# Kernel tuning notes

Hardware: AMD Instinct MI355X
Metric: run time of the kernel (lower is better)

The kernel has to match this reference:

```python
import jax, jax.numpy as jnp
import numpy as np

B, T, D, H = 2, 2048, 2048, 16
HD = D // H  # 128
HALF = HD // 2  # 64


def _apply_rotary(x, cos, sin):
    """x: (B,H,T,HD); cos/sin: (T, HD//2). Interleaved rotation matching torch ref."""
    half = x.shape[-1] // 2
    x1, x2 = x[..., :half], x[..., half:]
    c = cos[None, None, :, :]
    s = sin[None, None, :, :]
    # stack on last axis then flatten -> out[...,2i]=x1*c-x2*s, out[...,2i+1]=x1*s+x2*c
    return jnp.stack([x1 * c - x2 * s, x1 * s + x2 * c], axis=-1).reshape(x.shape)


def setup_inputs() -> dict:
    key = jax.random.key(0)
    k1, k2, k3 = jax.random.split(key, 3)
    x = jax.random.normal(k1, (B, T, D), dtype=jnp.float32)
    # realistic RoPE tables: theta = 10000^{-2i/HD}
    inv_freq = 1.0 / (10000.0 ** (np.arange(0, HALF, dtype=np.float32) * 2.0 / HD))
    ang = np.arange(T, dtype=np.float32)[:, None] * inv_freq[None, :]  # (T, HALF)
    cos = jnp.asarray(np.cos(ang), dtype=jnp.float32)
    sin = jnp.asarray(np.sin(ang), dtype=jnp.float32)
    Wqkv = jax.random.normal(k2, (D, 3 * D), dtype=jnp.float32) * (D ** -0.5)
    Wproj = jax.random.normal(k3, (D, D), dtype=jnp.float32) * (D ** -0.5)
    return {"x": x, "cos": cos, "sin": sin, "Wqkv": Wqkv, "Wproj": Wproj}


def reference(x, cos, sin, Wqkv, Wproj):
    b, t, d = x.shape
    qkv = (x @ Wqkv).reshape(b, t, 3, H, HD)
    q = jnp.transpose(qkv[:, :, 0], (0, 2, 1, 3))  # (B,H,T,HD)
    k = jnp.transpose(qkv[:, :, 1], (0, 2, 1, 3))
    v = jnp.transpose(qkv[:, :, 2], (0, 2, 1, 3))
    q = _apply_rotary(q, cos, sin)
    k = _apply_rotary(k, cos, sin)
    scale = 1.0 / jnp.sqrt(jnp.asarray(HD, dtype=x.dtype))
    scores = jnp.einsum("bhqd,bhkd->bhqk", q, k) * scale
    causal = jnp.tril(jnp.ones((t, t), dtype=bool))
    scores = jnp.where(causal[None, None], scores, jnp.finfo(x.dtype).min)
    attn = jax.nn.softmax(scores, axis=-1)
    out = jnp.einsum("bhqk,bhkd->bhqd", attn, v)
    out = jnp.transpose(out, (0, 2, 1, 3)).reshape(b, t, d)
    return out @ Wproj
```

## Files before the change

kernel.cpp:

```cpp
#include <hip/hip_runtime.h>
#include <hip/hip_bf16.h>

#define B_  2
#define T_  2048
#define D_  2048
#define H_  16
#define HD_ 128
#define NT_ 4096
#define D3_ 6144

typedef __bf16 bf16;
typedef _Float16 f16;
typedef bf16 bf16x2 __attribute__((ext_vector_type(2)));
typedef bf16 bf16x4 __attribute__((ext_vector_type(4)));
typedef bf16 bf16x8 __attribute__((ext_vector_type(8)));
typedef f16  f16x2  __attribute__((ext_vector_type(2)));
typedef f16  f16x4  __attribute__((ext_vector_type(4)));
typedef float floatx4 __attribute__((ext_vector_type(4)));

__device__ __forceinline__ void gl_lds16(const void* g, void* l) {
    __builtin_amdgcn_global_load_lds((const __attribute__((address_space(1))) void*)g,
                                     (__attribute__((address_space(3))) void*)l, 16, 0, 0);
}

__global__ __launch_bounds__(256) void k_prep(const float* __restrict__ x,
                                              const float* __restrict__ Wqkv, const float* __restrict__ Wproj,
                                              bf16* __restrict__ xb, bf16* __restrict__ WqkvT, bf16* __restrict__ WprojT) {
    int blk = blockIdx.x;
    int tid = threadIdx.x;
    if (blk < 8192) {
        int i = blk * 256 + tid;
        float4 v = ((const float4*)x)[i];
        bf16x4 o = { (bf16)v.x, (bf16)v.y, (bf16)v.z, (bf16)v.w };
        ((bf16x4*)xb)[i] = o;
        return;
    }
    __shared__ float tile[64][65];
    const float* in; bf16* out; int C, bx;
    if (blk < 8192 + 3072) { bx = blk - 8192; in = Wqkv; out = WqkvT; C = D3_; }
    else                   { bx = blk - 8192 - 3072; in = Wproj; out = WprojT; C = D_; }
    const int R = D_;
    int nbx = C / 64;
    int c0 = (bx % nbx) * 64, r0 = (bx / nbx) * 64;
#pragma unroll
    for (int i = 0; i < 16; i++) {
        int idx = tid + i * 256, r = idx >> 6, c = idx & 63;
        tile[r][c] = in[(size_t)(r0 + r) * C + (c0 + c)];
    }
    __syncthreads();
#pragma unroll
    for (int i = 0; i < 16; i++) {
        int idx = tid + i * 256, r = idx >> 6, c = idx & 63;
        out[(size_t)(c0 + r) * R + (r0 + c)] = (bf16)tile[c][r];
    }
}

__global__ __launch_bounds__(256) void k_gemm_qkv(const bf16* __restrict__ A, const bf16* __restrict__ Bt,
                                                  const float* __restrict__ cosp, const float* __restrict__ sinp,
                                                  bf16* __restrict__ Qg, bf16* __restrict__ Kg, f16* __restrict__ VTg) {
    __shared__ bf16 As[128 * 32];
    __shared__ bf16 Bs[128 * 32];
    __shared__ bf16 stage[128 * 130];
    const int tid = threadIdx.x, w = tid >> 6, lane = tid & 63;
    const int quad = lane >> 4, l16 = lane & 15;
    const int n0 = blockIdx.x * 128, m0 = blockIdx.y * 128;
    const int wr = (w >> 1) * 64, wc = (w & 1) * 64;
    const int srow = lane >> 2, schunk = (lane & 3) ^ ((lane >> 2) & 3);
    const bf16* Aw = A + (size_t)m0 * D_ + (size_t)(w * 32 + srow) * D_ + schunk * 8;
    const bf16* Bw = Bt + (size_t)n0 * D_ + (size_t)(w * 32 + srow) * D_ + schunk * 8;
    const int co = (quad ^ (l16 & 3)) * 8;
    const bf16* Abase = As + (wr + l16) * 32 + co;
    const bf16* Bbase = Bs + (wc + l16) * 32 + co;
    floatx4 acc[4][4] = {};
    for (int k0 = 0; k0 < D_; k0 += 32) {
        __syncthreads();
#pragma unroll
        for (int i = 0; i < 2; i++) {
            gl_lds16(Aw + k0 + i * 16 * D_, As + (w * 2 + i) * 512);
            gl_lds16(Bw + k0 + i * 16 * D_, Bs + (w * 2 + i) * 512);
        }
        __syncthreads();
        bf16x8 af[4], bfr[4];
#pragma unroll
        for (int mt = 0; mt < 4; mt++) af[mt] = *(const bf16x8*)(Abase + mt * 512);
#pragma unroll
        for (int nt = 0; nt < 4; nt++) bfr[nt] = *(const bf16x8*)(Bbase + nt * 512);
#pragma unroll
        for (int mt = 0; mt < 4; mt++)
#pragma unroll
            for (int nt = 0; nt < 4; nt++)
                acc[mt][nt] = __builtin_amdgcn_mfma_f32_16x16x32_bf16(af[mt], bfr[nt], acc[mt][nt], 0, 0, 0);
    }
    __syncthreads();
#pragma unroll
    for (int mt = 0; mt < 4; mt++)
#pragma unroll
        for (int nt = 0; nt < 4; nt++)
#pragma unroll
            for (int r = 0; r < 4; r++)
                stage[(wr + mt * 16 + quad * 4 + r) * 130 + wc + nt * 16 + l16] = (bf16)acc[mt][nt][r];
    __syncthreads();
    const int type = n0 >> 11, h = (n0 & 2047) >> 7;
    const int b = m0 >> 11, t0 = m0 & 2047;
    if (type < 2) {
        bf16* out = (type == 0 ? Qg : Kg) + ((size_t)(b * H_ + h) * T_ + t0) * HD_;
#pragma unroll
        for (int it = 0; it < 32; it++) {
            int idx = it * 256 + tid, tl = idx >> 6, i = idx & 63;
            float c = cosp[(t0 + tl) * 64 + i], s = sinp[(t0 + tl) * 64 + i];
            float x1 = (float)stage[tl * 130 + i], x2 = (float)stage[tl * 130 + 64 + i];
            bf16x2 o = { (bf16)(x1 * c - x2 * s), (bf16)(x1 * s + x2 * c) };
            *(bf16x2*)(out + (size_t)tl * HD_ + 2 * i) = o;
        }
    } else {
        f16* out = VTg + (size_t)(b * H_ + h) * HD_ * T_ + t0;
#pragma unroll
        for (int it = 0; it < 32; it++) {
            int idx = it * 256 + tid, d = idx >> 6, tp = (idx & 63) * 2;
            f16x2 o = { (f16)(float)stage[tp * 130 + d], (f16)(float)stage[(tp + 1) * 130 + d] };
            *(f16x2*)(out + (size_t)d * T_ + tp) = o;
        }
    }
}

template <typename OutT>
__global__ __launch_bounds__(256) void k_gemm_bt(const bf16* __restrict__ A, const bf16* __restrict__ Bt,
                                                 OutT* __restrict__ C, int M, int N, int K) {
    __shared__ bf16 As[128 * 64];
    __shared__ bf16 Bs[128 * 64];
    const int tid = threadIdx.x, w = tid >> 6, lane = tid & 63;
    const int quad = lane >> 4, l16 = lane & 15;
    const int x7 = l16 & 7;
    const int n0 = blockIdx.x * 128, m0 = blockIdx.y * 128;
    const int wr = (w >> 1) * 64, wc = (w & 1) * 64;
    const bf16* Ab = A + (size_t)m0 * K;
    const bf16* Bb = Bt + (size_t)n0 * K;
    const int srow = lane >> 3, schunk = (lane & 7) ^ (lane >> 3);
    floatx4 acc[4][4] = {};
    for (int k0 = 0; k0 < K; k0 += 64) {
        __syncthreads();
#pragma unroll
        for (int i = 0; i < 4; i++) {
            int ch = w * 4 + i;
            int row = ch * 8 + srow;
            gl_lds16(Ab + (size_t)row * K + k0 + schunk * 8, As + ch * 512);
            gl_lds16(Bb + (size_t)row * K + k0 + schunk * 8, Bs + ch * 512);
        }
        __syncthreads();
#pragma unroll
        for (int kc = 0; kc < 2; kc++) {
            const int co = ((kc * 4 + quad) ^ x7) * 8;
            const bf16* Abase = As + (wr + l16) * 64 + co;
            const bf16* Bbase = Bs + (wc + l16) * 64 + co;
            bf16x8 af[4], bfr[4];
#pragma unroll
            for (int mt = 0; mt < 4; mt++) af[mt] = *(const bf16x8*)(Abase + mt * 1024);
#pragma unroll
            for (int nt = 0; nt < 4; nt++) bfr[nt] = *(const bf16x8*)(Bbase + nt * 1024);
#pragma unroll
            for (int mt = 0; mt < 4; mt++)
#pragma unroll
                for (int nt = 0; nt < 4; nt++)
                    acc[mt][nt] = __builtin_amdgcn_mfma_f32_16x16x32_bf16(af[mt], bfr[nt], acc[mt][nt], 0, 0, 0);
        }
    }
#pragma unroll
    for (int mt = 0; mt < 4; mt++)
#pragma unroll
        for (int nt = 0; nt < 4; nt++)
#pragma unroll
            for (int r = 0; r < 4; r++) {
                int row = m0 + wr + mt * 16 + quad * 4 + r;
                int col = n0 + wc + nt * 16 + l16;
                C[(size_t)row * N + col] = (OutT)acc[mt][nt][r];
            }
}

__global__ __launch_bounds__(256, 2) void k_flash(const bf16* __restrict__ Qg, const bf16* __restrict__ Kg,
                                                  const f16* __restrict__ VTg, bf16* __restrict__ Og) {
    __shared__ bf16 Ksh[64 * 128];
    __shared__ f16  Vsh[128 * 64];
    const int b1 = blockIdx.x;
    const int bh = b1 & 31;
    const int qt = (b1 < 256) ? (15 - (b1 >> 5)) : ((b1 - 256) >> 5);
    const int tid = threadIdx.x, w = tid >> 6, lane = tid & 63;
    const int quad = lane >> 4, l16 = lane & 15;
    const float scale2 = 0.08838834764831845f * 1.4426950408889634f;
    const int wrow = w * 32;
    const bf16* Qb = Qg + ((size_t)bh * T_ + qt * 128) * HD_;
    bf16x8 qf[2][4];
#pragma unroll
    for (int mt = 0; mt < 2; mt++)
#pragma unroll
        for (int kc = 0; kc < 4; kc++)
            qf[mt][kc] = *(const bf16x8*)(Qb + (size_t)(wrow + mt * 16 + l16) * HD_ + kc * 32 + quad * 8);
    floatx4 oaccT[8][2] = {};
    float lsum[2] = { 0.f, 0.f };
    const int nkt = 2 * (qt + 1);
    for (int kt = 0; kt < nkt; kt++) {
        __syncthreads();
        const bf16* Kt = Kg + ((size_t)bh * T_ + kt * 64) * HD_;
        const f16*  Vt = VTg + (size_t)bh * HD_ * T_ + kt * 64;
#pragma unroll
        for (int i = 0; i < 4; i++) {
            int ch = w * 4 + i;
            {
                int row = ch * 4 + (lane >> 4);
                int c = (lane & 15) ^ (row & 7);
                gl_lds16(Kt + (size_t)row * HD_ + c * 8, Ksh + ch * 512);
            }
            {
                int row = ch * 8 + (lane >> 3);
                int c = (lane & 7) ^ (row & 7);
                gl_lds16(Vt + (size_t)row * T_ + c * 8, Vsh + ch * 512);
            }
        }
        __syncthreads();
        const bool diag = (kt >= 2 * qt);
        f16x4 pf[2][4];
#pragma unroll
        for (int nt = 0; nt < 4; nt++) {
            floatx4 s0 = {}, s1 = {};
#pragma unroll
            for (int kc = 0; kc < 4; kc++) {
                bf16x8 kf = *(const bf16x8*)(Ksh + (nt * 16 + l16) * 128 + (((kc * 4 + quad) ^ (l16 & 7)) * 8));
                s0 = __builtin_amdgcn_mfma_f32_16x16x32_bf16(kf, qf[0][kc], s0, 0, 0, 0);
                s1 = __builtin_amdgcn_mfma_f32_16x16x32_bf16(kf, qf[1][kc], s1, 0, 0, 0);
            }
#pragma unroll
            for (int r = 0; r < 4; r++) {
                float v0 = s0[r] * scale2, v1 = s1[r] * scale2;
                if (diag) {
                    int gk = kt * 64 + nt * 16 + quad * 4 + r;
                    if (gk > qt * 128 + wrow + l16) v0 = -1e30f;
                    if (gk > qt * 128 + wrow + 16 + l16) v1 = -1e30f;
                }
                float p0 = exp2f(v0), p1 = exp2f(v1);
                lsum[0] += p0; lsum[1] += p1;
                pf[0][nt][r] = (f16)p0; pf[1][nt][r] = (f16)p1;
            }
        }
#pragma unroll
        for (int nt = 0; nt < 4; nt++)
#pragma unroll
            for (int dt = 0; dt < 8; dt++) {
                int row = dt * 16 + l16;
                f16x4 vf = *(const f16x4*)(Vsh + row * 64 + (((nt * 2 + (quad >> 1)) ^ (row & 7)) * 8) + (quad & 1) * 4);
#pragma unroll
                for (int mt = 0; mt < 2; mt++)
                    oaccT[dt][mt] = __builtin_amdgcn_mfma_f32_16x16x16f16(vf, pf[mt][nt], oaccT[dt][mt], 0, 0, 0);
            }
    }
    const int b = bh >> 4, h = bh & 15;
    float inv[2];
#pragma unroll
    for (int mt = 0; mt < 2; mt++) {
        float l = lsum[mt];
        l += __shfl_xor(l, 16);
        l += __shfl_xor(l, 32);
        inv[mt] = 1.0f / l;
    }
#pragma unroll
    for (int mt = 0; mt < 2; mt++) {
        int t = qt * 128 + wrow + mt * 16 + l16;
#pragma unroll
        for (int dt = 0; dt < 8; dt++) {
            bf16x4 o;
#pragma unroll
            for (int r = 0; r < 4; r++) o[r] = (bf16)(oaccT[dt][mt][r] * inv[mt]);
            int c = h * HD_ + dt * 16 + quad * 4;
            *(bf16x4*)(Og + (size_t)(b * T_ + t) * D_ + c) = o;
        }
    }
}

extern "C" void kernel_launch(void* const* d_in, const int* in_sizes, int n_in,
                              void* d_out, int out_size, void* d_ws, size_t ws_size,
                              hipStream_t stream) {
    const float* x     = (const float*)d_in[0];
    const float* cosp  = (const float*)d_in[1];
    const float* sinp  = (const float*)d_in[2];
    const float* Wqkv  = (const float*)d_in[3];
    const float* Wproj = (const float*)d_in[4];
    float* out = (float*)d_out;
    char* ws = (char*)d_ws;
    bf16* xb     = (bf16*)(ws);
    bf16* WqkvT  = (bf16*)(ws + (size_t)(16u << 20));
    bf16* WprojT = (bf16*)(ws + (size_t)(40u << 20));
    bf16* Qg     = (bf16*)(ws + (size_t)(48u << 20));
    bf16* Kg     = (bf16*)(ws + (size_t)(64u << 20));
    f16*  VTg    = (f16*) (ws + (size_t)(80u << 20));
    bf16* Og     = xb;

    k_prep<<<dim3(8192 + 3072 + 1024), 256, 0, stream>>>(x, Wqkv, Wproj, xb, WqkvT, WprojT);
    k_gemm_qkv<<<dim3(D3_ / 128, NT_ / 128), 256, 0, stream>>>(xb, WqkvT, cosp, sinp, Qg, Kg, VTg);
    k_flash<<<dim3(512), 256, 0, stream>>>(Qg, Kg, VTg, Og);
    k_gemm_bt<float><<<dim3(D_ / 128, NT_ / 128), 256, 0, stream>>>(Og, WprojT, out, NT_, D_, D_);
}
```

Baseline: 375.4 us.

## Double-buffer K/V tiles in LDS to prefetch the next tile during compute

```diff
diff --git a/kernel.cpp b/kernel.cpp
--- a/kernel.cpp
+++ b/kernel.cpp
@@ -178,8 +178,8 @@
 
 __global__ __launch_bounds__(256, 2) void k_flash(const bf16* __restrict__ Qg, const bf16* __restrict__ Kg,
                                                   const f16* __restrict__ VTg, bf16* __restrict__ Og) {
-    __shared__ bf16 Ksh[64 * 128];
-    __shared__ f16  Vsh[128 * 64];
+    __shared__ bf16 Ksh[2][64 * 128];
+    __shared__ f16  Vsh[2][128 * 64];
     const int b1 = blockIdx.x;
     const int bh = b1 & 31;
     const int qt = (b1 < 256) ? (15 - (b1 >> 5)) : ((b1 - 256) >> 5);
@@ -187,6 +187,9 @@
     const int quad = lane >> 4, l16 = lane & 15;
     const float scale2 = 0.08838834764831845f * 1.4426950408889634f;
     const int wrow = w * 32;
+    const bf16* Kb = Kg + (size_t)bh * T_ * HD_;
+    const f16*  Vb = VTg + (size_t)bh * HD_ * T_;
+    const int krow_ = (lane >> 4), kc_ = (lane & 15) ^ 0;
     const bf16* Qb = Qg + ((size_t)bh * T_ + qt * 128) * HD_;
     bf16x8 qf[2][4];
 #pragma unroll
@@ -197,25 +200,49 @@
     floatx4 oaccT[8][2] = {};
     float lsum[2] = { 0.f, 0.f };
     const int nkt = 2 * (qt + 1);
-    for (int kt = 0; kt < nkt; kt++) {
-        __syncthreads();
-        const bf16* Kt = Kg + ((size_t)bh * T_ + kt * 64) * HD_;
-        const f16*  Vt = VTg + (size_t)bh * HD_ * T_ + kt * 64;
+
+    {
+        const bf16* Kt = Kb;
+        const f16*  Vt = Vb;
 #pragma unroll
         for (int i = 0; i < 4; i++) {
             int ch = w * 4 + i;
             {
                 int row = ch * 4 + (lane >> 4);
                 int c = (lane & 15) ^ (row & 7);
-                gl_lds16(Kt + (size_t)row * HD_ + c * 8, Ksh + ch * 512);
+                gl_lds16(Kt + (size_t)row * HD_ + c * 8, &Ksh[0][ch * 512]);
             }
             {
                 int row = ch * 8 + (lane >> 3);
                 int c = (lane & 7) ^ (row & 7);
-                gl_lds16(Vt + (size_t)row * T_ + c * 8, Vsh + ch * 512);
-            }
-        }
-        __syncthreads();
+                gl_lds16(Vt + (size_t)row * T_ + c * 8, &Vsh[0][ch * 512]);
+            }
+        }
+    }
+    int cur = 0;
+    for (int kt = 0; kt < nkt; kt++) {
+        __syncthreads();
+        if (kt + 1 < nkt) {
+            const bf16* Kt = Kb + (size_t)(kt + 1) * 64 * HD_;
+            const f16*  Vt = Vb + (size_t)(kt + 1) * 64;
+            const int nb = cur ^ 1;
+#pragma unroll
+            for (int i = 0; i < 4; i++) {
+                int ch = w * 4 + i;
+                {
+                    int row = ch * 4 + (lane >> 4);
+                    int c = (lane & 15) ^ (row & 7);
+                    gl_lds16(Kt + (size_t)row * HD_ + c * 8, &Ksh[nb][ch * 512]);
+                }
+                {
+                    int row = ch * 8 + (lane >> 3);
+                    int c = (lane & 7) ^ (row & 7);
+                    gl_lds16(Vt + (size_t)row * T_ + c * 8, &Vsh[nb][ch * 512]);
+                }
+            }
+        }
+        const bf16* Kcur = Ksh[cur];
+        const f16*  Vcur = Vsh[cur];
         const bool diag = (kt >= 2 * qt);
         f16x4 pf[2][4];
 #pragma unroll
@@ -223,7 +250,7 @@
             floatx4 s0 = {}, s1 = {};
 #pragma unroll
             for (int kc = 0; kc < 4; kc++) {
-                bf16x8 kf = *(const bf16x8*)(Ksh + (nt * 16 + l16) * 128 + (((kc * 4 + quad) ^ (l16 & 7)) * 8));
+                bf16x8 kf = *(const bf16x8*)(Kcur + (nt * 16 + l16) * 128 + (((kc * 4 + quad) ^ (l16 & 7)) * 8));
                 s0 = __builtin_amdgcn_mfma_f32_16x16x32_bf16(kf, qf[0][kc], s0, 0, 0, 0);
                 s1 = __builtin_amdgcn_mfma_f32_16x16x32_bf16(kf, qf[1][kc], s1, 0, 0, 0);
             }
@@ -245,11 +272,12 @@
 #pragma unroll
             for (int dt = 0; dt < 8; dt++) {
                 int row = dt * 16 + l16;
-                f16x4 vf = *(const f16x4*)(Vsh + row * 64 + (((nt * 2 + (quad >> 1)) ^ (row & 7)) * 8) + (quad & 1) * 4);
+                f16x4 vf = *(const f16x4*)(Vcur + row * 64 + (((nt * 2 + (quad >> 1)) ^ (row & 7)) * 8) + (quad & 1) * 4);
 #pragma unroll
                 for (int mt = 0; mt < 2; mt++)
                     oaccT[dt][mt] = __builtin_amdgcn_mfma_f32_16x16x16f16(vf, pf[mt][nt], oaccT[dt][mt], 0, 0, 0);
             }
+        cur ^= 1;
     }
     const int b = bh >> 4, h = bh & 15;
     float inv[2];
```

After: 379.2 us. Within noise of the previous version (+1.0%).
